# Optimization experiments

Measured on AMD Instinct MI355X. Metric: run time of the kernel, lower is better.

## Reference

```python
import jax, jax.numpy as jnp
import numpy as np

B, N, F = 4, 1024, 256
AVG_DEG = 16.0


def setup_inputs() -> dict:
    key = jax.random.key(0)
    k1, k2, k3, k4 = jax.random.split(key, 4)
    u = jax.random.uniform(k1, (B, N, N))
    A = (u < AVG_DEG / N).astype(jnp.float32)
    A = jnp.maximum(A, jnp.swapaxes(A, 1, 2))            # symmetric
    A = A * (1.0 - jnp.eye(N, dtype=jnp.float32))        # no self loops (added in forward)
    x = jax.random.normal(k2, (B, N, F), dtype=jnp.float32)
    pos = jax.random.normal(k3, (B, N, 3), dtype=jnp.float32)
    order = jax.random.uniform(k4, (B, N), dtype=jnp.float32)  # 'random' ordering priorities
    node_mask = jnp.ones((B, N), dtype=bool)
    return {"x": x, "adj": A, "pos": pos, "order": order, "node_mask": node_mask}


def _select(order, excluded, included, node_mask):
    # Greedy frontier-based node selection (K-MIS with stride=2).
    Bn, Nn = order.shape
    ar = jnp.arange(Nn)
    idx0 = jnp.argmin(order, axis=-1).astype(jnp.int32)           # [B]
    available = node_mask
    frontier = ar[None, :] == idx0[:, None]                        # scatter idx0 -> True
    selected = jnp.zeros_like(available)

    def cond(st):
        av, fr, sel, idx = st
        return av.any()

    def body(st):
        av, fr, sel, idx = st
        current = ar[None, :] == idx[:, None]                      # [B,N] one-hot
        sel = sel | current
        exc_row = jnp.take_along_axis(excluded, idx[:, None, None], axis=1)[:, 0]  # excluded[current]
        inc_row = jnp.take_along_axis(included, idx[:, None, None], axis=1)[:, 0]  # included[current]
        av = av & ~current & ~exc_row
        fr = (fr | inc_row | ~fr.any(-1, keepdims=True)) & av      # restart frontier if empty
        mo = jnp.where(fr, order, jnp.inf)
        midx = jnp.argmin(mo, axis=-1).astype(jnp.int32)
        has_fr = fr.any(-1)
        idx = jnp.where(has_fr, midx, idx)
        return (av, fr, sel, idx)

    _, _, selected, _ = jax.lax.while_loop(cond, body, (available, frontier, selected, idx0))
    return selected


def _forward(x, adj, pos, order, node_mask):
    Nn = adj.shape[1]
    eye = jnp.eye(Nn, dtype=adj.dtype)
    adj1 = jnp.where(node_mask[:, :, None], adj + eye, 0.0)        # adj_k[1] = A + I, masked rows
    adj2 = adj1 @ adj                                              # adj_k[2] = (A+I) @ A
    excluded = adj1 != 0                                           # adj_k[stride-1].bool()
    included = adj2 != 0                                           # adj_k[stride].bool()
    selected = _select(jax.lax.stop_gradient(order), excluded, included, node_mask)
    # pad K to N instead of data-dependent num_nodes; mask zeroes the padding
    mask_f, perm = jax.lax.top_k(selected.astype(jnp.float32), Nn)  # [B,K], [B,K]
    adj_kernel = jnp.take_along_axis(adj1, perm[:, None, :], axis=2)  # [B,N,K]
    # add_pool: adj^T @ x, then mask
    x_p = jnp.einsum('bnk,bnf->bkf', adj_kernel, x) * mask_f[..., None]
    # mean_pool for pos: add_pool / column degree
    deg = adj_kernel.sum(axis=1)[..., None]                        # [B,K,1]
    pos_p = jnp.einsum('bnk,bnc->bkc', adj_kernel, pos) / deg * mask_f[..., None]
    # coarsened adjacency: gather cols then rows of adj_k[stride], mask both sides
    a = jnp.take_along_axis(adj2, perm[:, None, :], axis=2)
    a = jnp.take_along_axis(a, perm[:, :, None], axis=1)
    a = a * mask_f[:, None, :] * mask_f[:, :, None]
    return x_p, pos_p, a, mask_f.astype(bool)


def reference(x, adj, pos, order, node_mask):
    return _forward(x, adj, pos, order, node_mask)
```

## Files before the change

kernel.cpp:

```cpp
#include <hip/hip_runtime.h>
#include <hip/hip_bf16.h>

#define BB 4
#define NN 1024
#define FF 256

typedef __hip_bfloat16 bf16;
typedef unsigned long long u64;
typedef unsigned int u32;
typedef unsigned char u8;

__device__ __forceinline__ bf16 f2b(float v) { return __float2bfloat16(v); }
__device__ __forceinline__ void stf(float* p, size_t i, float v) { p[i] = v; }
__device__ __forceinline__ void stf(bf16* p, size_t i, float v) { p[i] = f2b(v); }

__global__ __launch_bounds__(512) void pack_sort_kernel(const float* __restrict__ adj,
                                                        const float* __restrict__ order,
                                                        u64* __restrict__ bitsA,
                                                        int* __restrict__ sp2node,
                                                        int* __restrict__ node2sp) {
    const int b = blockIdx.y, t = threadIdx.x;
    __shared__ u64 keys[NN];
    if (blockIdx.x < NN) {
        const int r = blockIdx.x;
        const size_t base = (size_t)b * NN * NN + (size_t)r * NN;
        for (int i = 0; i < 2; i++) {
            int j = i * 512 + t;
            u64 bal = __ballot(adj[base + j] != 0.0f);
            if ((t & 63) == 0) bitsA[((size_t)b * NN + r) * 16 + (j >> 6)] = bal;
        }
        return;
    }
    for (int i = t; i < NN; i += 512) {
        float v = order[(size_t)b * NN + i];
        u32 ub = __float_as_uint(v);
        u32 sk = (ub & 0x80000000u) ? ~ub : (ub | 0x80000000u);
        keys[i] = ((u64)sk << 32) | (u32)i;
    }
    __syncthreads();
    for (int k = 2; k <= NN; k <<= 1) {
        for (int j = k >> 1; j > 0; j >>= 1) {
            for (int i = t; i < NN; i += 512) {
                int ixj = i ^ j;
                if (ixj > i) {
                    bool up = (i & k) == 0;
                    u64 a = keys[i], c = keys[ixj];
                    if ((a > c) == up) { keys[i] = c; keys[ixj] = a; }
                }
            }
            __syncthreads();
        }
    }
    for (int i = t; i < NN; i += 512) {
        int n = (int)(keys[i] & 0xFFFFFFFFu);
        sp2node[b * NN + i] = n;
        node2sp[b * NN + n] = i;
    }
}

__global__ void inc_pack_kernel(const u64* __restrict__ bitsA,
                                const int* __restrict__ sp2node,
                                const int* __restrict__ node2sp,
                                u32* __restrict__ packed) {
    const int r = blockIdx.x, b = blockIdx.y, t = threadIdx.x;
    __shared__ u64 myrow[16], incw[16];
    __shared__ u64 part[256];
    __shared__ unsigned short nbr[192];
    __shared__ int s2nT[NN];
    __shared__ int cnt;
    if (t == 0) cnt = 0;
    if (t < 16) myrow[t] = bitsA[((size_t)b * NN + r) * 16 + t];
    __syncthreads();
    for (int i = 0; i < 4; i++) {
        int j = i * 256 + t;
        if ((myrow[j >> 6] >> (j & 63)) & 1) {
            int p = atomicAdd(&cnt, 1);
            if (p < 192) nbr[p] = (unsigned short)j;
        }
        s2nT[(j & 15) * 64 + (j >> 4)] = sp2node[b * NN + j];
    }
    __syncthreads();
    const int c = min(cnt, 192);
    {
        const int w = t & 15, g = t >> 4;
        u64 v = 0;
        for (int n = g; n < c; n += 16)
            v |= bitsA[((size_t)b * NN + nbr[n]) * 16 + w];
        part[t] = v;
    }
    __syncthreads();
    if (t < 16) {
        u64 acc = myrow[t];
        for (int g = 0; g < 16; g++) acc |= part[g * 16 + t];
        incw[t] = acc;
    }
    __syncthreads();
    if (t < 64) {
        const int s = node2sp[b * NN + r];
        u32 e16 = 0, i16 = 0;
        for (int q = 0; q < 16; q++) {
            int jn = s2nT[q * 64 + t];
            u32 eb = (u32)((myrow[jn >> 6] >> (jn & 63)) & 1) | (u32)(jn == r);
            u32 ib = (u32)((incw[jn >> 6] >> (jn & 63)) & 1);
            e16 |= eb << q;
            i16 |= ib << q;
        }
        packed[((size_t)b * NN + s) * 64 + t] = e16 | (i16 << 16);
    }
}

__global__ __launch_bounds__(256) void select_kernel(const u32* __restrict__ packed,
                                                     const int* __restrict__ node2sp,
                                                     int* __restrict__ perm,
                                                     int* __restrict__ kcount,
                                                     int* __restrict__ sink) {
    const int b = blockIdx.x, t = threadIdx.x;
    __shared__ u8 selS[NN];

    const uint4* pp = (const uint4*)(packed + (size_t)b * NN * 64);
    u32 acc = 0;
    for (int i = t; i < NN * 16; i += 256) {
        uint4 v = pp[i];
        acc ^= v.x ^ v.y ^ v.z ^ v.w;
    }
    if (acc == 0xDEADBEEFu) atomicAdd(sink, 1);
    __syncthreads();

    if (t < 64) {
        const int l = t;
        u32 avail = 0xFFFFu, front = (l == 0) ? 1u : 0u, sel = 0u;
        int cur = 0;
        for (int iter = 0; iter < 2 * NN + 8; ++iter) {
            if ((cur >> 4) == l) sel |= 1u << (cur & 15);
            u32 p = packed[((size_t)b * NN + cur) * 64 + l];
            avail &= ~(p & 0xFFFFu);
            front = (front | (p >> 16)) & avail;
            u64 fb = __ballot(front != 0u);
            if (!fb) {
                front = avail;
                fb = __ballot(front != 0u);
                if (!fb) break;
            }
            int lf = __ffsll(fb) - 1;
            u32 f = __shfl(front, lf);
            cur = lf * 16 + (__ffs(f) - 1);
        }
        for (int q = 0; q < 16; q++) selS[l * 16 + q] = (sel >> q) & 1u;
    }
    __syncthreads();

    if (t < 64) {
        const int l = t;
        u32 nodesel = 0;
        const int* n2s = node2sp + b * NN;
        for (int q = 0; q < 16; q++)
            nodesel |= ((u32)selS[n2s[l * 16 + q]]) << q;

        int cnt_sel = __popc(nodesel);
        int ps = cnt_sel;
        for (int off = 1; off < 64; off <<= 1) {
            int v = __shfl_up(ps, off);
            if (l >= off) ps += v;
        }
        const int K = __shfl(ps, 63);
        int pos = ps - cnt_sel;
        u32 m = nodesel;
        while (m) { int i = __ffs(m) - 1; perm[b * NN + pos++] = l * 16 + i; m &= m - 1; }
        int posu = K + l * 16 - (ps - cnt_sel);
        m = (~nodesel) & 0xFFFFu;
        while (m) { int i = __ffs(m) - 1; perm[b * NN + posu++] = l * 16 + i; m &= m - 1; }
        if (l == 0) kcount[b] = K;
    }
}

template <typename OUT>
__global__ void fused_out_kernel(const u64* __restrict__ bitsA, const float* __restrict__ x,
                                 const float* __restrict__ pos,
                                 const int* __restrict__ perm, const int* __restrict__ kcount,
                                 OUT* __restrict__ out_x, OUT* __restrict__ out_pos,
                                 OUT* __restrict__ out_a, OUT* __restrict__ out_mask) {
    const int k = blockIdx.x, b = blockIdx.y, t = threadIdx.x;
    const int K = kcount[b];
    OUT* ox = out_x + ((size_t)b * NN + k) * FF;
    OUT* op = out_pos + ((size_t)b * NN + k) * 3;
    OUT* oa = out_a + ((size_t)b * NN + k) * NN;
    if (t == 0) stf(out_mask, (size_t)b * NN + k, k < K ? 1.0f : 0.0f);
    if (k >= K) {
        stf(ox, t, 0.0f);
        if (t < 3) stf(op, t, 0.0f);
        for (int q = 0; q < 4; q++) stf(oa, t + q * 256, 0.0f);
        return;
    }
    const int r = perm[b * NN + k];
    __shared__ int p[NN];
    __shared__ u64 myrow[16];
    __shared__ unsigned short nbr[192];
    __shared__ int cnt;
    if (t == 0) cnt = 0;
    if (t < 16) myrow[t] = bitsA[((size_t)b * NN + r) * 16 + t];
    for (int q = 0; q < 4; q++) { int j = t + q * 256; p[j] = perm[b * NN + j]; }
    __syncthreads();
    for (int i = 0; i < 4; i++) {
        int j = i * 256 + t;
        if ((myrow[j >> 6] >> (j & 63)) & 1) {
            int pp = atomicAdd(&cnt, 1);
            if (pp < 192) nbr[pp] = (unsigned short)j;
        }
    }
    __syncthreads();
    const int c = min(cnt, 192);

    const size_t xb = (size_t)b * NN * FF;
    float acc = x[xb + (size_t)r * FF + t];
    for (int n = 0; n < c; n++) acc += x[xb + (size_t)nbr[n] * FF + t];
    stf(ox, t, acc);
    if (t < 3) {
        const size_t pb = (size_t)b * NN * 3;
        float pa = pos[pb + r * 3 + t];
        for (int n = 0; n < c; n++) pa += pos[pb + nbr[n] * 3 + t];
        stf(op, t, pa / (float)(c + 1));
    }

    for (int q = 0; q < 4; q++) {
        int jj = t + q * 256;
        float v = 0.0f;
        if (jj < K) {
            const int pj = p[jj];
            const u64* rj = bitsA + ((size_t)b * NN + pj) * 16;
            int a2 = (int)((myrow[pj >> 6] >> (pj & 63)) & 1);
#pragma unroll
            for (int w = 0; w < 16; w++)
                a2 += __popcll(myrow[w] & rj[w]);
            v = (float)a2;
        }
        stf(oa, jj, v);
    }
}

extern "C" void kernel_launch(void* const* d_in, const int* in_sizes, int n_in,
                              void* d_out, int out_size, void* d_ws, size_t ws_size,
                              hipStream_t stream) {
    const float* x     = (const float*)d_in[0];
    const float* adj   = (const float*)d_in[1];
    const float* pos   = (const float*)d_in[2];
    const float* order = (const float*)d_in[3];

    char* ws = (char*)d_ws;
    size_t off = 0;
    u64* bitsA   = (u64*)(ws + off); off += (size_t)BB * NN * 16 * 8;
    u32* packed  = (u32*)(ws + off); off += (size_t)BB * NN * 64 * 4;
    int* sp2node = (int*)(ws + off); off += (size_t)BB * NN * 4;
    int* node2sp = (int*)(ws + off); off += (size_t)BB * NN * 4;
    int* perm    = (int*)(ws + off); off += (size_t)BB * NN * 4;
    int* kcnt    = (int*)(ws + off); off += BB * 4;
    int* sink    = (int*)(ws + off);

    bool outf32 = false;
    size_t osz = 0;
    if (hipMemPtrGetInfo(d_out, &osz) == hipSuccess)
        outf32 = (osz >= 4ull * (size_t)out_size);

    pack_sort_kernel<<<dim3(NN + 1, BB), 512, 0, stream>>>(adj, order, bitsA, sp2node, node2sp);
    inc_pack_kernel<<<dim3(NN, BB), 256, 0, stream>>>(bitsA, sp2node, node2sp, packed);
    select_kernel<<<BB, 256, 0, stream>>>(packed, node2sp, perm, kcnt, sink);

    if (outf32) {
        float* out      = (float*)d_out;
        float* out_x    = out;
        float* out_pos  = out_x + (size_t)BB * NN * FF;
        float* out_a    = out_pos + (size_t)BB * NN * 3;
        float* out_mask = out_a + (size_t)BB * NN * NN;
        fused_out_kernel<float><<<dim3(NN, BB), 256, 0, stream>>>(bitsA, x, pos, perm, kcnt,
                                                                  out_x, out_pos, out_a, out_mask);
    } else {
        bf16* out      = (bf16*)d_out;
        bf16* out_x    = out;
        bf16* out_pos  = out_x + (size_t)BB * NN * FF;
        bf16* out_a    = out_pos + (size_t)BB * NN * 3;
        bf16* out_mask = out_a + (size_t)BB * NN * NN;
        fused_out_kernel<bf16><<<dim3(NN, BB), 256, 0, stream>>>(bitsA, x, pos, perm, kcnt,
                                                                 out_x, out_pos, out_a, out_mask);
    }
}
```

Before: 151.7 us.

## Rank-sort order keys, pad LDS transpose, stage bf16 outputs for vector stores

Replaces the shared-memory bitonic sort of ordering keys with a rank-by-counting pass, so each thread computes the final positions of its two keys without the many barrier-separated stages. Pads the transposed sp2node table in LDS from a stride of 64 to 65 to avoid bank conflicts. Splits the output kernel into f32 and bf16 versions. The bf16 version stages the x and adjacency rows in shared memory and writes them with 16-byte vector stores, including the zero fill for padded rows. The rank sort does O(N) LDS reads per thread, which could cost more than the bitonic network, and it relies on the keys being unique.

```diff
diff --git a/kernel.cpp b/kernel.cpp
--- a/kernel.cpp
+++ b/kernel.cpp
@@ -8,9 +8,15 @@
 typedef __hip_bfloat16 bf16;
 typedef unsigned long long u64;
 typedef unsigned int u32;
+typedef unsigned short u16;
 typedef unsigned char u8;
 
 __device__ __forceinline__ bf16 f2b(float v) { return __float2bfloat16(v); }
+__device__ __forceinline__ u16 f2bbits(float v) {
+    bf16 h = __float2bfloat16(v);
+    u16 s; __builtin_memcpy(&s, &h, 2);
+    return s;
+}
 __device__ __forceinline__ void stf(float* p, size_t i, float v) { p[i] = v; }
 __device__ __forceinline__ void stf(bf16* p, size_t i, float v) { p[i] = f2b(v); }
 
@@ -38,23 +44,17 @@
         keys[i] = ((u64)sk << 32) | (u32)i;
     }
     __syncthreads();
-    for (int k = 2; k <= NN; k <<= 1) {
-        for (int j = k >> 1; j > 0; j >>= 1) {
-            for (int i = t; i < NN; i += 512) {
-                int ixj = i ^ j;
-                if (ixj > i) {
-                    bool up = (i & k) == 0;
-                    u64 a = keys[i], c = keys[ixj];
-                    if ((a > c) == up) { keys[i] = c; keys[ixj] = a; }
-                }
-            }
-            __syncthreads();
-        }
-    }
-    for (int i = t; i < NN; i += 512) {
-        int n = (int)(keys[i] & 0xFFFFFFFFu);
-        sp2node[b * NN + i] = n;
-        node2sp[b * NN + n] = i;
+    {
+        u64 mk0 = keys[t], mk1 = keys[t + 512];
+        int r0 = 0, r1 = 0;
+        for (int m = 0; m < NN; m++) {
+            u64 v = keys[m];
+            r0 += (v < mk0);
+            r1 += (v < mk1);
+        }
+        int n0 = (int)(mk0 & 0xFFFFFFFFu), n1 = (int)(mk1 & 0xFFFFFFFFu);
+        sp2node[b * NN + r0] = n0; node2sp[b * NN + n0] = r0;
+        sp2node[b * NN + r1] = n1; node2sp[b * NN + n1] = r1;
     }
 }
 
@@ -66,7 +66,7 @@
     __shared__ u64 myrow[16], incw[16];
     __shared__ u64 part[256];
     __shared__ unsigned short nbr[192];
-    __shared__ int s2nT[NN];
+    __shared__ int s2nT[16 * 65];
     __shared__ int cnt;
     if (t == 0) cnt = 0;
     if (t < 16) myrow[t] = bitsA[((size_t)b * NN + r) * 16 + t];
@@ -77,7 +77,7 @@
             int p = atomicAdd(&cnt, 1);
             if (p < 192) nbr[p] = (unsigned short)j;
         }
-        s2nT[(j & 15) * 64 + (j >> 4)] = sp2node[b * NN + j];
+        s2nT[(j & 15) * 65 + (j >> 4)] = sp2node[b * NN + j];
     }
     __syncthreads();
     const int c = min(cnt, 192);
@@ -99,7 +99,7 @@
         const int s = node2sp[b * NN + r];
         u32 e16 = 0, i16 = 0;
         for (int q = 0; q < 16; q++) {
-            int jn = s2nT[q * 64 + t];
+            int jn = s2nT[q * 65 + t];
             u32 eb = (u32)((myrow[jn >> 6] >> (jn & 63)) & 1) | (u32)(jn == r);
             u32 ib = (u32)((incw[jn >> 6] >> (jn & 63)) & 1);
             e16 |= eb << q;
@@ -173,28 +173,31 @@
     }
 }
 
-template <typename OUT>
-__global__ void fused_out_kernel(const u64* __restrict__ bitsA, const float* __restrict__ x,
+__global__ __launch_bounds__(256) void fused_out_bf16(const u64* __restrict__ bitsA,
+                                 const float* __restrict__ x,
                                  const float* __restrict__ pos,
                                  const int* __restrict__ perm, const int* __restrict__ kcount,
-                                 OUT* __restrict__ out_x, OUT* __restrict__ out_pos,
-                                 OUT* __restrict__ out_a, OUT* __restrict__ out_mask) {
+                                 bf16* __restrict__ out_x, bf16* __restrict__ out_pos,
+                                 bf16* __restrict__ out_a, bf16* __restrict__ out_mask) {
     const int k = blockIdx.x, b = blockIdx.y, t = threadIdx.x;
     const int K = kcount[b];
-    OUT* ox = out_x + ((size_t)b * NN + k) * FF;
-    OUT* op = out_pos + ((size_t)b * NN + k) * 3;
-    OUT* oa = out_a + ((size_t)b * NN + k) * NN;
-    if (t == 0) stf(out_mask, (size_t)b * NN + k, k < K ? 1.0f : 0.0f);
+    bf16* ox = out_x + ((size_t)b * NN + k) * FF;
+    bf16* op = out_pos + ((size_t)b * NN + k) * 3;
+    bf16* oa = out_a + ((size_t)b * NN + k) * NN;
+    if (t == 0) out_mask[(size_t)b * NN + k] = f2b(k < K ? 1.0f : 0.0f);
     if (k >= K) {
-        stf(ox, t, 0.0f);
-        if (t < 3) stf(op, t, 0.0f);
-        for (int q = 0; q < 4; q++) stf(oa, t + q * 256, 0.0f);
+        uint4 z = make_uint4(0, 0, 0, 0);
+        if (t < 128) ((uint4*)oa)[t] = z;
+        if (t < 32)  ((uint4*)ox)[t] = z;
+        if (t < 3) op[t] = f2b(0.0f);
         return;
     }
     const int r = perm[b * NN + k];
     __shared__ int p[NN];
     __shared__ u64 myrow[16];
     __shared__ unsigned short nbr[192];
+    __shared__ u16 stx[FF];
+    __shared__ u16 sta[NN];
     __shared__ int cnt;
     if (t == 0) cnt = 0;
     if (t < 16) myrow[t] = bitsA[((size_t)b * NN + r) * 16 + t];
@@ -213,12 +216,12 @@
     const size_t xb = (size_t)b * NN * FF;
     float acc = x[xb + (size_t)r * FF + t];
     for (int n = 0; n < c; n++) acc += x[xb + (size_t)nbr[n] * FF + t];
-    stf(ox, t, acc);
+    stx[t] = f2bbits(acc);
     if (t < 3) {
         const size_t pb = (size_t)b * NN * 3;
         float pa = pos[pb + r * 3 + t];
         for (int n = 0; n < c; n++) pa += pos[pb + nbr[n] * 3 + t];
-        stf(op, t, pa / (float)(c + 1));
+        op[t] = f2b(pa / (float)(c + 1));
     }
 
     for (int q = 0; q < 4; q++) {
@@ -233,7 +236,71 @@
                 a2 += __popcll(myrow[w] & rj[w]);
             v = (float)a2;
         }
-        stf(oa, jj, v);
+        sta[jj] = f2bbits(v);
+    }
+    __syncthreads();
+    if (t < 128) ((uint4*)oa)[t] = ((const uint4*)sta)[t];
+    if (t < 32)  ((uint4*)ox)[t] = ((const uint4*)stx)[t];
+}
+
+__global__ void fused_out_f32(const u64* __restrict__ bitsA, const float* __restrict__ x,
+                              const float* __restrict__ pos,
+                              const int* __restrict__ perm, const int* __restrict__ kcount,
+                              float* __restrict__ out_x, float* __restrict__ out_pos,
+                              float* __restrict__ out_a, float* __restrict__ out_mask) {
+    const int k = blockIdx.x, b = blockIdx.y, t = threadIdx.x;
+    const int K = kcount[b];
+    float* ox = out_x + ((size_t)b * NN + k) * FF;
+    float* op = out_pos + ((size_t)b * NN + k) * 3;
+    float* oa = out_a + ((size_t)b * NN + k) * NN;
+    if (t == 0) out_mask[(size_t)b * NN + k] = k < K ? 1.0f : 0.0f;
+    if (k >= K) {
+        ox[t] = 0.0f;
+        if (t < 3) op[t] = 0.0f;
+        for (int q = 0; q < 4; q++) oa[t + q * 256] = 0.0f;
+        return;
+    }
+    const int r = perm[b * NN + k];
+    __shared__ int p[NN];
+    __shared__ u64 myrow[16];
+    __shared__ unsigned short nbr[192];
+    __shared__ int cnt;
+    if (t == 0) cnt = 0;
+    if (t < 16) myrow[t] = bitsA[((size_t)b * NN + r) * 16 + t];
+    for (int q = 0; q < 4; q++) { int j = t + q * 256; p[j] = perm[b * NN + j]; }
+    __syncthreads();
+    for (int i = 0; i < 4; i++) {
+        int j = i * 256 + t;
+        if ((myrow[j >> 6] >> (j & 63)) & 1) {
+            int pp = atomicAdd(&cnt, 1);
+            if (pp < 192) nbr[pp] = (unsigned short)j;
+        }
+    }
+    __syncthreads();
+    const int c = min(cnt, 192);
+    const size_t xb = (size_t)b * NN * FF;
+    float acc = x[xb + (size_t)r * FF + t];
+    for (int n = 0; n < c; n++) acc += x[xb + (size_t)nbr[n] * FF + t];
+    ox[t] = acc;
+    if (t < 3) {
+        const size_t pb = (size_t)b * NN * 3;
+        float pa = pos[pb + r * 3 + t];
+        for (int n = 0; n < c; n++) pa += pos[pb + nbr[n] * 3 + t];
+        op[t] = pa / (float)(c + 1);
+    }
+    for (int q = 0; q < 4; q++) {
+        int jj = t + q * 256;
+        float v = 0.0f;
+        if (jj < K) {
+            const int pj = p[jj];
+            const u64* rj = bitsA + ((size_t)b * NN + pj) * 16;
+            int a2 = (int)((myrow[pj >> 6] >> (pj & 63)) & 1);
+#pragma unroll
+            for (int w = 0; w < 16; w++)
+                a2 += __popcll(myrow[w] & rj[w]);
+            v = (float)a2;
+        }
+        oa[jj] = v;
     }
 }
 
@@ -270,15 +337,15 @@
         float* out_pos  = out_x + (size_t)BB * NN * FF;
         float* out_a    = out_pos + (size_t)BB * NN * 3;
         float* out_mask = out_a + (size_t)BB * NN * NN;
-        fused_out_kernel<float><<<dim3(NN, BB), 256, 0, stream>>>(bitsA, x, pos, perm, kcnt,
-                                                                  out_x, out_pos, out_a, out_mask);
+        fused_out_f32<<<dim3(NN, BB), 256, 0, stream>>>(bitsA, x, pos, perm, kcnt,
+                                                        out_x, out_pos, out_a, out_mask);
     } else {
         bf16* out      = (bf16*)d_out;
         bf16* out_x    = out;
         bf16* out_pos  = out_x + (size_t)BB * NN * FF;
         bf16* out_a    = out_pos + (size_t)BB * NN * 3;
         bf16* out_mask = out_a + (size_t)BB * NN * NN;
-        fused_out_kernel<bf16><<<dim3(NN, BB), 256, 0, stream>>>(bitsA, x, pos, perm, kcnt,
-                                                                 out_x, out_pos, out_a, out_mask);
-    }
-}
+        fused_out_bf16<<<dim3(NN, BB), 256, 0, stream>>>(bitsA, x, pos, perm, kcnt,
+                                                         out_x, out_pos, out_a, out_mask);
+    }
+}
```

New measurement: 151.7 us, median of 2. About the same (-0.0%).
